# Performance work log

Hardware: AMD Instinct MI355X
Metric: run time of the kernel (lower is better)

Reference implementation:

```python
import jax, jax.numpy as jnp
import numpy as np
import math

B, C, A, W, H = 8, 128, 16, 64, 64


def setup_inputs() -> dict:
    key = jax.random.key(0)
    ks = jax.random.split(key, 7)
    s_in = 1.0 / math.sqrt(C)
    return {
        "x": jax.random.normal(ks[0], (B, C, W, H), dtype=jnp.float32),
        "Wq": jax.random.normal(ks[1], (A, C), dtype=jnp.float32) * s_in,
        "bq": jnp.zeros((A,), dtype=jnp.float32),
        "Wk": jax.random.normal(ks[2], (A, C), dtype=jnp.float32) * s_in,
        "bk": jnp.zeros((A,), dtype=jnp.float32),
        "Wv": jax.random.normal(ks[3], (C, C), dtype=jnp.float32) * s_in,
        "bv": jnp.zeros((C,), dtype=jnp.float32),
    }


def reference(x, Wq, bq, Wk, bk, Wv, bv):
    # 1x1 convs == per-pixel linear projections
    q = jnp.einsum('ac,bcwh->bawh', Wq, x) + bq[None, :, None, None]  # [B,A,W,H]
    k = jnp.einsum('ac,bcwh->bawh', Wk, x) + bk[None, :, None, None]  # [B,A,W,H]
    v = jnp.einsum('vc,bcwh->bvwh', Wv, x) + bv[None, :, None, None]  # [B,C,W,H]

    scale = 1.0 / math.sqrt(q.shape[1])
    # full spatial attention: [B, W, H, W, H]
    attn = jnp.einsum('bawh,baWH->bwhWH', q, k)
    b, w, h, _, _ = attn.shape
    attn = jax.nn.softmax(attn.reshape(b, w, h, -1) * scale, axis=-1)
    attn = attn.reshape(b, w, h, w, h)
    out = jnp.einsum('bwhWH,bvWH->bvwh', attn, v)  # [B,C,W,H]
    return out
```

## Files before the change

### kernel.cpp

```cpp
#include <hip/hip_runtime.h>
#include <math.h>

#define BB 8
#define CC 128
#define NN 4096

typedef _Float16 f16;
typedef _Float16 f16x4v __attribute__((ext_vector_type(4)));
typedef _Float16 f16x8 __attribute__((ext_vector_type(8)));
typedef float f32x4v __attribute__((ext_vector_type(4)));
typedef float f32x16 __attribute__((ext_vector_type(16)));

#if __has_builtin(__builtin_amdgcn_exp2f)
#define EXP2(x) __builtin_amdgcn_exp2f(x)
#else
#define EXP2(x) __expf((x)*0.69314718056f)
#endif

#define QSCALE 0.360673760222f
#define SHIFT  5.770780163555f

#define WF_BYTES 65536

__global__ __launch_bounds__(256)
void prep_kernel(const float* __restrict__ Wq, const float* __restrict__ bq,
                 const float* __restrict__ Wk, const float* __restrict__ bk,
                 const float* __restrict__ Wv, const float* __restrict__ bv,
                 f16* __restrict__ Wf, float* __restrict__ biasS)
{
    const int tg = blockIdx.x*256 + threadIdx.x;
    if (tg < 2560) {
        const int mt = tg >> 9, ks = (tg >> 6) & 7, l = tg & 63;
        const int n32 = l & 31, h = l >> 5;
        const int r = mt*32 + n32;
        f16x8 v8;
        #pragma unroll
        for (int i = 0; i < 8; i++) {
            int c = ks*16 + 8*h + i;
            float wv_;
            if (r < 16)      wv_ = QSCALE * Wq[r*CC + c];
            else if (r < 32) wv_ = Wk[(r-16)*CC + c];
            else             wv_ = Wv[(r-32)*CC + c];
            v8[i] = (f16)wv_;
        }
        *(f16x8*)&Wf[(size_t)tg*8] = v8;
    }
    if (blockIdx.x == 0 && threadIdx.x < 160) {
        int r = threadIdx.x;
        biasS[r] = r < 16 ? QSCALE*bq[r] : (r < 32 ? bk[r-16] : bv[r-32]);
    }
}

__global__ __launch_bounds__(256)
void proj_kernel(const float* __restrict__ x, const f16* __restrict__ Wf,
                 const float* __restrict__ biasS,
                 f16* __restrict__ Qt, f16* __restrict__ Kt, f16* __restrict__ Vf)
{
    __shared__ __align__(16) f16 Vl[CC*140];

    const int tid  = threadIdx.x;
    const int lane = tid & 63;
    const int wv   = tid >> 6;
    const int b    = blockIdx.x & 7;
    const int pt   = blockIdx.x >> 3;
    const int n32  = lane & 31;
    const int half = lane >> 5;
    const int p    = pt*128 + wv*32 + n32;

    const float* xp = x + (size_t)b*CC*NN + p;
    f16x8 xf[8];
    #pragma unroll
    for (int ks = 0; ks < 8; ks++) {
        float xv[8];
        #pragma unroll
        for (int i = 0; i < 8; i++)
            xv[i] = __builtin_nontemporal_load(&xp[(size_t)(ks*16 + 8*half + i)*NN]);
        #pragma unroll
        for (int i = 0; i < 8; i++) xf[ks][i] = (f16)xv[i];
    }

    f32x16 acc[5];
    #pragma unroll
    for (int mt = 0; mt < 5; mt++) acc[mt] = (f32x16)0.0f;
    #pragma unroll
    for (int ks = 0; ks < 8; ks++) {
        #pragma unroll
        for (int mt = 0; mt < 5; mt++) {
            f16x8 wfr = *(const f16x8*)&Wf[((size_t)(mt*8 + ks)*64 + lane)*8];
            acc[mt] = __builtin_amdgcn_mfma_f32_32x32x16_f16(wfr, xf[ks], acc[mt], 0, 0, 0);
        }
    }

    #pragma unroll
    for (int mt = 0; mt < 5; mt++) {
        #pragma unroll
        for (int q = 0; q < 4; q++) {
            float4 b4 = *(const float4*)&biasS[mt*32 + q*8 + 4*half];
            acc[mt][q*4+0] += b4.x; acc[mt][q*4+1] += b4.y;
            acc[mt][q*4+2] += b4.z; acc[mt][q*4+3] += b4.w;
        }
    }

    {
        size_t qkoff = ((size_t)b*NN + p)*16;
        f16x4v s0, s1, s2, s3;
        #pragma unroll
        for (int i = 0; i < 4; i++) {
            s0[i] = (f16)acc[0][i];    s1[i] = (f16)acc[0][4+i];
            s2[i] = (f16)acc[0][8+i];  s3[i] = (f16)acc[0][12+i];
        }
        *(f16x4v*)&Qt[qkoff + 4*half]     = s0;
        *(f16x4v*)&Qt[qkoff + 8 + 4*half] = s1;
        *(f16x4v*)&Kt[qkoff + 4*half]     = s2;
        *(f16x4v*)&Kt[qkoff + 8 + 4*half] = s3;
    }

    #pragma unroll
    for (int mt = 1; mt < 5; mt++) {
        #pragma unroll
        for (int g = 0; g < 16; g++) {
            int c = (mt-1)*32 + (g & 3) + 8*(g >> 2) + 4*half;
            Vl[c*140 + wv*32 + n32] = (f16)acc[mt][g];
        }
    }
    __syncthreads();

    #pragma unroll
    for (int pass = 0; pass < 8; pass++) {
        int item = pass*256 + tid;
        int l    = item & 63;
        int f    = (item >> 6) & 15;
        int ktl  = item >> 10;
        int c16  = f >> 2, ct = f & 3;
        int li   = l & 31, h2 = l >> 5;
        const f16* src = &Vl[(ct*32 + li)*140 + ktl*64 + c16*16 + 4*h2];
        f16x4v lo = *(const f16x4v*)&src[0];
        f16x4v hi = *(const f16x4v*)&src[8];
        f16x8 v8;
        #pragma unroll
        for (int i = 0; i < 4; i++) { v8[i] = lo[i]; v8[4+i] = hi[i]; }
        int ktg = pt*2 + ktl;
        *(f16x8*)&Vf[((((size_t)b*64 + ktg)*16 + c16*4 + ct)*64 + l)*8] = v8;
    }
}

__global__ __launch_bounds__(256, 2)
void attn_kernel(const f16* __restrict__ Qt, const f16* __restrict__ Kt,
                 const f16* __restrict__ Vf, float* __restrict__ out)
{
    __shared__ __align__(16) unsigned char lds_raw[53504];

    const int tid  = threadIdx.x;
    const int lane = tid & 63;
    const int wv   = tid >> 6;
    const int cp   = wv & 1;
    const int kh   = wv >> 1;
    const int b    = blockIdx.x & 7;
    const int qt   = blockIdx.x >> 3;
    const int q0   = qt*64;
    const int n32  = lane & 31;
    const int half = lane >> 5;

    const f16* vb = Vf + (size_t)b*64*16*512;
    const f16* kb = Kt + (size_t)b*NN*16;
    const f16x8 qfA = *(const f16x8*)&Qt[((size_t)b*NN + q0 + n32)*16 + half*8];
    const f16x8 qfB = *(const f16x8*)&Qt[((size_t)b*NN + q0 + 32 + n32)*16 + half*8];

    f32x16 ofA[2], ofB[2];
    #pragma unroll
    for (int c = 0; c < 2; c++) { ofA[c] = (f32x16)0.0f; ofB[c] = (f32x16)0.0f; }
    float psA[4] = {0.f, 0.f, 0.f, 0.f};
    float psB[4] = {0.f, 0.f, 0.f, 0.f};

    f16x8 kf0 = *(const f16x8*)&kb[((size_t)kh*64 + n32)*16 + half*8];
    f16x8 kf1 = *(const f16x8*)&kb[((size_t)kh*64 + 32 + n32)*16 + half*8];
    f16x8 vpf[8];
    {
        const f16* vt = vb + (size_t)kh*8192;
        #pragma unroll
        for (int kc = 0; kc < 4; kc++)
            #pragma unroll
            for (int j = 0; j < 2; j++)
                vpf[kc*2+j] = *(const f16x8*)&vt[((size_t)(kc*4 + 2*cp + j)*64 + lane)*8];
    }

    for (int kt = kh; kt < NN/64; kt += 2) {
        const int ktn = (kt + 2 < NN/64) ? kt + 2 : kt;
        f16x8 kf0n = *(const f16x8*)&kb[((size_t)ktn*64 + n32)*16 + half*8];
        f16x8 kf1n = *(const f16x8*)&kb[((size_t)ktn*64 + 32 + n32)*16 + half*8];

        f16x8 pfA[4];
        {
            f32x16 St0 = __builtin_amdgcn_mfma_f32_32x32x16_f16(kf0, qfA, (f32x16)(-SHIFT), 0, 0, 0);
            f32x16 St1 = __builtin_amdgcn_mfma_f32_32x32x16_f16(kf1, qfA, (f32x16)(-SHIFT), 0, 0, 0);
            #pragma unroll
            for (int g = 0; g < 16; g++) {
                float e0 = EXP2(St0[g]); psA[g & 3] += e0; pfA[(g >> 3)][g & 7]     = (f16)e0;
                float e1 = EXP2(St1[g]); psA[g & 3] += e1; pfA[2 + (g >> 3)][g & 7] = (f16)e1;
            }
        }
        f16x8 pfB[4];
        {
            f32x16 St0 = __builtin_amdgcn_mfma_f32_32x32x16_f16(kf0, qfB, (f32x16)(-SHIFT), 0, 0, 0);
            f32x16 St1 = __builtin_amdgcn_mfma_f32_32x32x16_f16(kf1, qfB, (f32x16)(-SHIFT), 0, 0, 0);
            #pragma unroll
            for (int g = 0; g < 16; g++) {
                float e0 = EXP2(St0[g]); psB[g & 3] += e0; pfB[(g >> 3)][g & 7]     = (f16)e0;
                float e1 = EXP2(St1[g]); psB[g & 3] += e1; pfB[2 + (g >> 3)][g & 7] = (f16)e1;
            }
        }

        const f16* vtn = vb + (size_t)ktn*8192;
        #pragma unroll
        for (int kc = 0; kc < 4; kc++) {
            #pragma unroll
            for (int j = 0; j < 2; j++) {
                const int ii = kc*2 + j;
                f16x8 vc = vpf[ii];
                vpf[ii] = *(const f16x8*)&vtn[((size_t)(kc*4 + 2*cp + j)*64 + lane)*8];
                ofA[j] = __builtin_amdgcn_mfma_f32_32x32x16_f16(pfA[kc], vc, ofA[j], 0, 0, 0);
                ofB[j] = __builtin_amdgcn_mfma_f32_32x32x16_f16(pfB[kc], vc, ofB[j], 0, 0, 0);
            }
        }
        kf0 = kf0n; kf1 = kf1n;
    }

    float lsA = (psA[0] + psA[1]) + (psA[2] + psA[3]);
    lsA += __shfl_xor(lsA, 32);
    float lsB = (psB[0] + psB[1]) + (psB[2] + psB[3]);
    lsB += __shfl_xor(lsB, 32);

    __syncthreads();
    if (wv >= 2) {
        unsigned char* base = lds_raw + (size_t)cp*9216 + (size_t)lane*144;
        #pragma unroll
        for (int a = 0; a < 4; a++) {
            #pragma unroll
            for (int h = 0; h < 2; h++) {
                f16x8 t;
                #pragma unroll
                for (int jj = 0; jj < 8; jj++)
                    t[jj] = (f16)((a < 2 ? ofA[a & 1] : ofB[a & 1])[h*8 + jj]);
                *(f16x8*)(base + a*32 + h*16) = t;
            }
        }
        *(float*)(base + 128) = lsA;
        *(float*)(base + 132) = lsB;
    }
    __syncthreads();
    if (wv < 2) {
        unsigned char* base = lds_raw + (size_t)cp*9216 + (size_t)lane*144;
        #pragma unroll
        for (int a = 0; a < 4; a++) {
            #pragma unroll
            for (int h = 0; h < 2; h++) {
                f16x8 t = *(const f16x8*)(base + a*32 + h*16);
                #pragma unroll
                for (int jj = 0; jj < 8; jj++) {
                    float v = (float)t[jj];
                    if (a < 2) ofA[a & 1][h*8 + jj] += v;
                    else       ofB[a & 1][h*8 + jj] += v;
                }
            }
        }
        if (wv == 0) {
            float lsA2 = *(const float*)(base + 128);
            float lsB2 = *(const float*)(base + 132);
            float* ls_inv = (float*)(lds_raw + 18432);
            if (lane < 32) {
                ls_inv[n32]      = 1.f / (lsA + lsA2);
                ls_inv[32 + n32] = 1.f / (lsB + lsB2);
            }
        }
    }
    __syncthreads();

    if (wv < 2) {
        const float* ls_inv = (const float*)(lds_raw + 18432);
        float* Tb = (float*)(lds_raw + 18688);
        #pragma unroll
        for (int qts = 0; qts < 2; qts++) {
            #pragma unroll
            for (int j = 0; j < 4; j++) {
                f32x4v iv = *(const f32x4v*)&ls_inv[qts*32 + 8*j + 4*half];
                #pragma unroll
                for (int ctl = 0; ctl < 2; ctl++) {
                    const int c = (2*cp + ctl)*32 + n32;
                    f32x4v o;
                    #pragma unroll
                    for (int e = 0; e < 4; e++)
                        o[e] = (qts ? ofB[ctl] : ofA[ctl])[4*j + e] * iv[e];
                    *(f32x4v*)&Tb[(size_t)c*68 + qts*32 + 8*j + 4*half] = o;
                }
            }
        }
    }
    __syncthreads();
    {
        const float* Tb = (const float*)(lds_raw + 18688);
        #pragma unroll
        for (int it = 0; it < 8; it++) {
            int idx = it*256 + tid;
            int c = idx >> 4, qg = idx & 15;
            f32x4v v = *(const f32x4v*)&Tb[(size_t)c*68 + qg*4];
            __builtin_nontemporal_store(v,
                (f32x4v*)&out[((size_t)b*CC + c)*NN + q0 + qg*4]);
        }
    }
}

extern "C" void kernel_launch(void* const* d_in, const int* in_sizes, int n_in,
                              void* d_out, int out_size, void* d_ws, size_t ws_size,
                              hipStream_t stream) {
    const float* x  = (const float*)d_in[0];
    const float* Wq = (const float*)d_in[1];
    const float* bq = (const float*)d_in[2];
    const float* Wk = (const float*)d_in[3];
    const float* bk = (const float*)d_in[4];
    const float* Wv = (const float*)d_in[5];
    const float* bv = (const float*)d_in[6];
    float* out = (float*)d_out;

    f16* Qw = (f16*)d_ws;
    f16* Kw = Qw + (size_t)BB*NN*16;
    f16* Vw = Kw + (size_t)BB*NN*16;
    unsigned char* tail = (unsigned char*)d_out + (size_t)out_size*4 - WF_BYTES;
    f16*   Wf    = (f16*)tail;
    float* biasS = (float*)(tail + 49152);

    hipLaunchKernelGGL(prep_kernel, dim3(10), dim3(256), 0, stream,
                       Wq, bq, Wk, bk, Wv, bv, Wf, biasS);
    hipLaunchKernelGGL(proj_kernel, dim3(256), dim3(256), 0, stream,
                       x, Wf, biasS, Qw, Kw, Vw);
    hipLaunchKernelGGL(attn_kernel, dim3(512), dim3(256), 0, stream,
                       Qw, Kw, Vw, out);
}
```

Before: 139.1 us.

## Split QK softmax between wave pairs and exchange P tiles through LDS

Previously every wave computed the score tiles and exponentials for both 32-query halves, so the QK MFMAs and exp work were duplicated across the two channel-pair waves. Now each wave computes P for only its own query half (selected by cp) and swaps it with its partner wave through a double-buffered LDS region. Both waves then run the full PV MFMAs. The exchange adds a block-wide __syncthreads in every iteration of the key loop, plus LDS traffic, which can stall waves that previously ran independently.

```diff
diff --git a/kernel.cpp b/kernel.cpp
--- a/kernel.cpp
+++ b/kernel.cpp
@@ -152,9 +152,9 @@
 
     const int tid  = threadIdx.x;
     const int lane = tid & 63;
-    const int wv   = tid >> 6;
-    const int cp   = wv & 1;
-    const int kh   = wv >> 1;
+    const int w    = tid >> 6;
+    const int cp   = w & 1;
+    const int kh   = w >> 1;
     const int b    = blockIdx.x & 7;
     const int qt   = blockIdx.x >> 3;
     const int q0   = qt*64;
@@ -163,14 +163,12 @@
 
     const f16* vb = Vf + (size_t)b*64*16*512;
     const f16* kb = Kt + (size_t)b*NN*16;
-    const f16x8 qfA = *(const f16x8*)&Qt[((size_t)b*NN + q0 + n32)*16 + half*8];
-    const f16x8 qfB = *(const f16x8*)&Qt[((size_t)b*NN + q0 + 32 + n32)*16 + half*8];
+    const f16x8 qf = *(const f16x8*)&Qt[((size_t)b*NN + q0 + cp*32 + n32)*16 + half*8];
 
     f32x16 ofA[2], ofB[2];
     #pragma unroll
     for (int c = 0; c < 2; c++) { ofA[c] = (f32x16)0.0f; ofB[c] = (f32x16)0.0f; }
-    float psA[4] = {0.f, 0.f, 0.f, 0.f};
-    float psB[4] = {0.f, 0.f, 0.f, 0.f};
+    float ps[4] = {0.f, 0.f, 0.f, 0.f};
 
     f16x8 kf0 = *(const f16x8*)&kb[((size_t)kh*64 + n32)*16 + half*8];
     f16x8 kf1 = *(const f16x8*)&kb[((size_t)kh*64 + 32 + n32)*16 + half*8];
@@ -184,54 +182,65 @@
                 vpf[kc*2+j] = *(const f16x8*)&vt[((size_t)(kc*4 + 2*cp + j)*64 + lane)*8];
     }
 
+    f16* Pex = (f16*)lds_raw;
+    int pb = 0;
+
     for (int kt = kh; kt < NN/64; kt += 2) {
         const int ktn = (kt + 2 < NN/64) ? kt + 2 : kt;
         f16x8 kf0n = *(const f16x8*)&kb[((size_t)ktn*64 + n32)*16 + half*8];
         f16x8 kf1n = *(const f16x8*)&kb[((size_t)ktn*64 + 32 + n32)*16 + half*8];
 
-        f16x8 pfA[4];
+        f16x8 po[4];
         {
-            f32x16 St0 = __builtin_amdgcn_mfma_f32_32x32x16_f16(kf0, qfA, (f32x16)(-SHIFT), 0, 0, 0);
-            f32x16 St1 = __builtin_amdgcn_mfma_f32_32x32x16_f16(kf1, qfA, (f32x16)(-SHIFT), 0, 0, 0);
+            f32x16 St0 = __builtin_amdgcn_mfma_f32_32x32x16_f16(kf0, qf, (f32x16)(-SHIFT), 0, 0, 0);
+            f32x16 St1 = __builtin_amdgcn_mfma_f32_32x32x16_f16(kf1, qf, (f32x16)(-SHIFT), 0, 0, 0);
             #pragma unroll
             for (int g = 0; g < 16; g++) {
-                float e0 = EXP2(St0[g]); psA[g & 3] += e0; pfA[(g >> 3)][g & 7]     = (f16)e0;
-                float e1 = EXP2(St1[g]); psA[g & 3] += e1; pfA[2 + (g >> 3)][g & 7] = (f16)e1;
+                float e0 = EXP2(St0[g]); ps[g & 3] += e0; po[(g >> 3)][g & 7]     = (f16)e0;
+                float e1 = EXP2(St1[g]); ps[g & 3] += e1; po[2 + (g >> 3)][g & 7] = (f16)e1;
             }
         }
-        f16x8 pfB[4];
+
         {
-            f32x16 St0 = __builtin_amdgcn_mfma_f32_32x32x16_f16(kf0, qfB, (f32x16)(-SHIFT), 0, 0, 0);
-            f32x16 St1 = __builtin_amdgcn_mfma_f32_32x32x16_f16(kf1, qfB, (f32x16)(-SHIFT), 0, 0, 0);
-            #pragma unroll
-            for (int g = 0; g < 16; g++) {
-                float e0 = EXP2(St0[g]); psB[g & 3] += e0; pfB[(g >> 3)][g & 7]     = (f16)e0;
-                float e1 = EXP2(St1[g]); psB[g & 3] += e1; pfB[2 + (g >> 3)][g & 7] = (f16)e1;
-            }
+            f16* wr = &Pex[((size_t)(w*2 + pb)*4*64 + lane)*8];
+            #pragma unroll
+            for (int kc = 0; kc < 4; kc++)
+                *(f16x8*)&wr[kc*512] = po[kc];
+        }
+        __syncthreads();
+        f16x8 pq[4];
+        {
+            const f16* rd = &Pex[((size_t)((w^1)*2 + pb)*4*64 + lane)*8];
+            #pragma unroll
+            for (int kc = 0; kc < 4; kc++)
+                pq[kc] = *(const f16x8*)&rd[kc*512];
         }
 
         const f16* vtn = vb + (size_t)ktn*8192;
-        #pragma unroll
-        for (int kc = 0; kc < 4; kc++) {
-            #pragma unroll
-            for (int j = 0; j < 2; j++) {
-                const int ii = kc*2 + j;
-                f16x8 vc = vpf[ii];
-                vpf[ii] = *(const f16x8*)&vtn[((size_t)(kc*4 + 2*cp + j)*64 + lane)*8];
-                ofA[j] = __builtin_amdgcn_mfma_f32_32x32x16_f16(pfA[kc], vc, ofA[j], 0, 0, 0);
-                ofB[j] = __builtin_amdgcn_mfma_f32_32x32x16_f16(pfB[kc], vc, ofB[j], 0, 0, 0);
-            }
-        }
-        kf0 = kf0n; kf1 = kf1n;
-    }
-
-    float lsA = (psA[0] + psA[1]) + (psA[2] + psA[3]);
-    lsA += __shfl_xor(lsA, 32);
-    float lsB = (psB[0] + psB[1]) + (psB[2] + psB[3]);
-    lsB += __shfl_xor(lsB, 32);
-
-    __syncthreads();
-    if (wv >= 2) {
+#define PV_BLOCK(PA, PB)                                                              \
+        _Pragma("unroll")                                                             \
+        for (int kc = 0; kc < 4; kc++) {                                              \
+            _Pragma("unroll")                                                         \
+            for (int j = 0; j < 2; j++) {                                             \
+                const int ii = kc*2 + j;                                              \
+                f16x8 vc = vpf[ii];                                                   \
+                vpf[ii] = *(const f16x8*)&vtn[((size_t)(kc*4 + 2*cp + j)*64 + lane)*8]; \
+                ofA[j] = __builtin_amdgcn_mfma_f32_32x32x16_f16(PA[kc], vc, ofA[j], 0, 0, 0); \
+                ofB[j] = __builtin_amdgcn_mfma_f32_32x32x16_f16(PB[kc], vc, ofB[j], 0, 0, 0); \
+            }                                                                         \
+        }
+        if (cp == 0) { PV_BLOCK(po, pq) }
+        else         { PV_BLOCK(pq, po) }
+#undef PV_BLOCK
+
+        kf0 = kf0n; kf1 = kf1n; pb ^= 1;
+    }
+
+    float ls = (ps[0] + ps[1]) + (ps[2] + ps[3]);
+    ls += __shfl_xor(ls, 32);
+
+    __syncthreads();
+    if (w >= 2) {
         unsigned char* base = lds_raw + (size_t)cp*9216 + (size_t)lane*144;
         #pragma unroll
         for (int a = 0; a < 4; a++) {
@@ -244,11 +253,10 @@
                 *(f16x8*)(base + a*32 + h*16) = t;
             }
         }
-        *(float*)(base + 128) = lsA;
-        *(float*)(base + 132) = lsB;
-    }
-    __syncthreads();
-    if (wv < 2) {
+        *(float*)(base + 128) = ls;
+    }
+    __syncthreads();
+    if (w < 2) {
         unsigned char* base = lds_raw + (size_t)cp*9216 + (size_t)lane*144;
         #pragma unroll
         for (int a = 0; a < 4; a++) {
@@ -263,19 +271,13 @@
                 }
             }
         }
-        if (wv == 0) {
-            float lsA2 = *(const float*)(base + 128);
-            float lsB2 = *(const float*)(base + 132);
-            float* ls_inv = (float*)(lds_raw + 18432);
-            if (lane < 32) {
-                ls_inv[n32]      = 1.f / (lsA + lsA2);
-                ls_inv[32 + n32] = 1.f / (lsB + lsB2);
-            }
-        }
-    }
-    __syncthreads();
-
-    if (wv < 2) {
+        ls += *(const float*)(base + 128);
+        float* ls_inv = (float*)(lds_raw + 18432);
+        if (lane < 32) ls_inv[cp*32 + n32] = 1.f / ls;
+    }
+    __syncthreads();
+
+    if (w < 2) {
         const float* ls_inv = (const float*)(lds_raw + 18432);
         float* Tb = (float*)(lds_raw + 18688);
         #pragma unroll
```

Measured after the change: 133.9 us. -3.7%, faster.
